# Kernel tuning notes

Hardware: AMD Instinct MI355X
Metric: run time of the kernel (lower is better)

Reference implementation:

```python
import jax, jax.numpy as jnp
import numpy as np

HIDDEN = 256
MAX_LENGTH = 256
NUM_LAYERS = 4
VOCAB = 50257


def setup_inputs() -> dict:
    key = jax.random.key(0)
    ks = jax.random.split(key, 16)
    s = 0.05
    return {
        "token": jax.random.randint(ks[0], (1,), 0, VOCAB, dtype=jnp.int64 if jax.config.jax_enable_x64 else jnp.int32),
        "hidden": jax.random.normal(ks[1], (NUM_LAYERS, 1, HIDDEN), dtype=jnp.float32),
        "encoder_outputs": jax.random.normal(ks[2], (MAX_LENGTH, HIDDEN), dtype=jnp.float32),
        "emb": jax.random.normal(ks[3], (VOCAB, HIDDEN), dtype=jnp.float32) * s,
        "attn_w": jax.random.normal(ks[4], (MAX_LENGTH, 2 * HIDDEN), dtype=jnp.float32) * s,
        "attn_b": jax.random.normal(ks[5], (MAX_LENGTH,), dtype=jnp.float32) * s,
        "comb_w": jax.random.normal(ks[6], (HIDDEN, 2 * HIDDEN), dtype=jnp.float32) * s,
        "comb_b": jax.random.normal(ks[7], (HIDDEN,), dtype=jnp.float32) * s,
        "gru_wih": jax.random.normal(ks[8], (NUM_LAYERS, 3 * HIDDEN, HIDDEN), dtype=jnp.float32) * s,
        "gru_whh": jax.random.normal(ks[9], (NUM_LAYERS, 3 * HIDDEN, HIDDEN), dtype=jnp.float32) * s,
        "gru_bih": jax.random.normal(ks[10], (NUM_LAYERS, 3 * HIDDEN), dtype=jnp.float32) * s,
        "gru_bhh": jax.random.normal(ks[11], (NUM_LAYERS, 3 * HIDDEN), dtype=jnp.float32) * s,
        "out_w": jax.random.normal(ks[12], (VOCAB, HIDDEN), dtype=jnp.float32) * s,
        "out_b": jax.random.normal(ks[13], (VOCAB,), dtype=jnp.float32) * s,
    }


def _gru_cell(x, h, wih, whh, bih, bhh):
    # PyTorch GRU cell: gates ordered [r, z, n]
    gi = x @ wih.T + bih  # [1, 3H]
    gh = h @ whh.T + bhh  # [1, 3H]
    i_r, i_z, i_n = jnp.split(gi, 3, axis=1)
    h_r, h_z, h_n = jnp.split(gh, 3, axis=1)
    r = jax.nn.sigmoid(i_r + h_r)
    z = jax.nn.sigmoid(i_z + h_z)
    n = jnp.tanh(i_n + r * h_n)
    return (1.0 - z) * n + z * h


def reference(token, hidden, encoder_outputs, emb, attn_w, attn_b, comb_w, comb_b,
              gru_wih, gru_whh, gru_bih, gru_bhh, out_w, out_b):
    # embedding lookup (dropout is identity in eval)  -> [1, H]
    embedded = emb[token]
    # Bahdanau-style attention weights over MAX_LENGTH positions
    attn_in = jnp.concatenate([embedded, hidden[0]], axis=1)  # [1, 2H]
    attn_weights = jax.nn.softmax(attn_in @ attn_w.T + attn_b, axis=1)  # [1, L]
    attn_applied = attn_weights @ encoder_outputs  # [1, H]
    comb_in = jnp.concatenate([embedded, attn_applied], axis=1)  # [1, 2H]
    x = jax.nn.relu(comb_in @ comb_w.T + comb_b)  # [1, H]
    # 4-layer GRU, single timestep
    new_h = []
    for l in range(NUM_LAYERS):
        h_l = _gru_cell(x, hidden[l], gru_wih[l], gru_whh[l], gru_bih[l], gru_bhh[l])
        new_h.append(h_l)
        x = h_l
    hidden_new = jnp.stack(new_h, axis=0)  # [4, 1, H]
    logp = jax.nn.log_softmax(x @ out_w.T + out_b, axis=1)  # [1, V]
    return (logp, hidden_new, attn_weights)
```

## Files before the change

### kernel.cpp

```cpp
#include <hip/hip_runtime.h>
#include <hip/hip_bf16.h>

#define H 256
#define L2H 512
#define NLAYERS 4
#define VOCAB 50257

#define OUT_LOGP 0
#define OUT_HID  50257
#define OUT_ATTN 51281

#define WS_SCORE  0
#define WS_BARS   256
#define WS_APP    512
#define WS_X0     768
#define WS_X1     1024
#define WS_PM     1280
#define WS_PS     1792
#define WS_FLAG   2304

#define NBLK 256
#define NGRP 16

typedef unsigned short u16;

__device__ __forceinline__ float bf2f(u16 u) {
    return __uint_as_float(((unsigned int)u) << 16);
}

__device__ __forceinline__ u16 f2bf(float f) {
    unsigned int x = __float_as_uint(f);
    unsigned int r = x + 0x7fff + ((x >> 16) & 1);
    return (u16)(r >> 16);
}

template<bool BF16>
__device__ __forceinline__ float ld1(const void* p, size_t i) {
    if (BF16) return bf2f(((const u16*)p)[i]);
    else      return ((const float*)p)[i];
}

template<bool BF16>
__device__ __forceinline__ float4 ld4(const void* p, size_t i) {
    if (BF16) {
        ushort4 w = *(const ushort4*)((const u16*)p + i);
        return make_float4(bf2f(w.x), bf2f(w.y), bf2f(w.z), bf2f(w.w));
    } else {
        return *(const float4*)((const float*)p + i);
    }
}

template<bool BF16>
__device__ __forceinline__ void ld8(const void* p, size_t i, float* f) {
    if (BF16) {
        uint4 u = *(const uint4*)((const u16*)p + i);
        f[0] = bf2f(u.x & 0xffff); f[1] = bf2f(u.x >> 16);
        f[2] = bf2f(u.y & 0xffff); f[3] = bf2f(u.y >> 16);
        f[4] = bf2f(u.z & 0xffff); f[5] = bf2f(u.z >> 16);
        f[6] = bf2f(u.w & 0xffff); f[7] = bf2f(u.w >> 16);
    } else {
        const float4* q = (const float4*)((const float*)p + i);
        float4 a = q[0], b = q[1];
        f[0] = a.x; f[1] = a.y; f[2] = a.z; f[3] = a.w;
        f[4] = b.x; f[5] = b.y; f[6] = b.z; f[7] = b.w;
    }
}

template<bool BF16>
__device__ __forceinline__ void st(void* p, size_t i, float v) {
    if (BF16) ((u16*)p)[i] = f2bf(v);
    else      ((float*)p)[i] = v;
}

__device__ __forceinline__ float ldc(const float* p) {
    return __hip_atomic_load(const_cast<float*>(p), __ATOMIC_RELAXED, __HIP_MEMORY_SCOPE_AGENT);
}
__device__ __forceinline__ void stc(float* p, float v) {
    __hip_atomic_store(p, v, __ATOMIC_RELAXED, __HIP_MEMORY_SCOPE_AGENT);
}

__device__ __forceinline__ void gbar(unsigned* bars, int i, bool arrive, unsigned exp) {
    __syncthreads();
    if (arrive && threadIdx.x == 0)
        __hip_atomic_fetch_add(&bars[(blockIdx.x & (NGRP - 1)) * 16 + i], 1u,
                               __ATOMIC_RELAXED, __HIP_MEMORY_SCOPE_AGENT);
    if (threadIdx.x < NGRP) {
        while (__hip_atomic_load(&bars[threadIdx.x * 16 + i],
                                 __ATOMIC_RELAXED, __HIP_MEMORY_SCOPE_AGENT) < exp)
            __builtin_amdgcn_s_sleep(1);
    }
    __syncthreads();
}

__global__ __launch_bounds__(256) void k_init(const void* emb, float* ws) {
    int tid = threadIdx.x;
    ((unsigned*)(ws + WS_BARS))[tid] = 0u;
    ws[WS_APP + tid] = 0.f;
    if (tid < 64) {
        float b = fabsf(bf2f(((const u16*)emb)[tid]));
        #pragma unroll
        for (int off = 32; off; off >>= 1) b = fmaxf(b, __shfl_xor(b, off));
        if (tid == 0) ws[WS_FLAG] = (b < 1.0f) ? 1.0f : 0.0f;
    }
}

template<bool BF16>
__device__ __forceinline__ void pipeline(
    const int* __restrict__ tok, const void* __restrict__ emb,
    const void* __restrict__ hidden,
    const void* __restrict__ attn_w, const void* __restrict__ attn_b,
    const void* __restrict__ enc,
    const void* __restrict__ comb_w, const void* __restrict__ comb_b,
    const void* __restrict__ gwih, const void* __restrict__ gwhh,
    const void* __restrict__ gbih, const void* __restrict__ gbhh,
    const void* __restrict__ out_w, const void* __restrict__ out_b,
    float* __restrict__ ws, void* __restrict__ out)
{
    unsigned* bars = (unsigned*)(ws + WS_BARS);
    const int tid  = threadIdx.x;
    const int lane = tid & 63;
    const int wid  = tid >> 6;
    const int bx   = blockIdx.x;
    const size_t es = BF16 ? 2 : 4;

    __shared__ float lds[256];
    __shared__ float wsm[256];

    if (bx < 64) {
        const int wv = (bx << 2) | wid;
        const int j8 = lane * 8;

        {
            float xin[8];
            if (lane < 32) ld8<BF16>(emb, (size_t)tok[0] * H + j8, xin);
            else           ld8<BF16>(hidden, (size_t)(j8 - H), xin);
            float wf[8]; ld8<BF16>(attn_w, (size_t)wv * L2H + j8, wf);
            float v = 0.f;
            #pragma unroll
            for (int q = 0; q < 8; ++q) v += xin[q] * wf[q];
            #pragma unroll
            for (int off = 32; off; off >>= 1) v += __shfl_xor(v, off);
            if (lane == 0) stc(ws + WS_SCORE + wv, v + ld1<BF16>(attn_b, wv));
        }
        gbar(bars, 0, true, 4);

        if (bx < 16) {
            float s = ldc(ws + WS_SCORE + tid);
            lds[tid] = s; __syncthreads();
            for (int off = 128; off; off >>= 1) {
                if (tid < off) lds[tid] = fmaxf(lds[tid], lds[tid + off]);
                __syncthreads();
            }
            float M = lds[0]; __syncthreads();
            float e = __expf(s - M);
            lds[tid] = e; __syncthreads();
            for (int off = 128; off; off >>= 1) {
                if (tid < off) lds[tid] += lds[tid + off];
                __syncthreads();
            }
            float w = e / lds[0];
            wsm[tid] = w; __syncthreads();
            if (bx == 0) st<BF16>(out, OUT_ATTN + tid, w);
            int l0 = bx * 16;
            float acc = 0.f;
            #pragma unroll
            for (int k = 0; k < 16; ++k)
                acc += wsm[l0 + k] * ld1<BF16>(enc, (size_t)(l0 + k) * H + tid);
            atomicAdd(&ws[WS_APP + tid], acc);
        }
        gbar(bars, 1, true, 4);

        {
            float xin[8];
            if (lane < 32) {
                ld8<BF16>(emb, (size_t)tok[0] * H + j8, xin);
            } else {
                #pragma unroll
                for (int q = 0; q < 8; ++q) xin[q] = ldc(ws + WS_APP + (j8 - H) + q);
            }
            float wf[8]; ld8<BF16>(comb_w, (size_t)wv * L2H + j8, wf);
            float v = 0.f;
            #pragma unroll
            for (int q = 0; q < 8; ++q) v += xin[q] * wf[q];
            #pragma unroll
            for (int off = 32; off; off >>= 1) v += __shfl_xor(v, off);
            if (lane == 0) stc(ws + WS_X0 + wv, fmaxf(v + ld1<BF16>(comb_b, wv), 0.f));
        }
        gbar(bars, 2, true, 4);

        const int e4 = lane * 4;
        for (int l = 0; l < NLAYERS; ++l) {
            const float* xin_p = ws + ((l & 1) ? WS_X1 : WS_X0);
            float*       xout  = ws + ((l & 1) ? WS_X0 : WS_X1);
            const char* wih = (const char*)gwih + (size_t)l * 3 * H * H * es;
            const char* whh = (const char*)gwhh + (size_t)l * 3 * H * H * es;
            const char* bih = (const char*)gbih + (size_t)l * 3 * H * es;
            const char* bhh = (const char*)gbhh + (size_t)l * 3 * H * es;
            const char* hprev = (const char*)hidden + (size_t)l * H * es;
            char*       hout  = (char*)out + (size_t)(OUT_HID + l * H) * es;

            float4 xv;
            xv.x = ldc(xin_p + e4);     xv.y = ldc(xin_p + e4 + 1);
            xv.z = ldc(xin_p + e4 + 2); xv.w = ldc(xin_p + e4 + 3);
            float4 hv = ld4<BF16>(hprev, e4);
            const int i = wv;

            float4 wri = ld4<BF16>(wih, (size_t)(i        ) * H + e4);
            float4 wzi = ld4<BF16>(wih, (size_t)(H + i    ) * H + e4);
            float4 wni = ld4<BF16>(wih, (size_t)(2 * H + i) * H + e4);
            float4 wrh = ld4<BF16>(whh, (size_t)(i        ) * H + e4);
            float4 wzh = ld4<BF16>(whh, (size_t)(H + i    ) * H + e4);
            float4 wnh = ld4<BF16>(whh, (size_t)(2 * H + i) * H + e4);

            float a = wri.x * xv.x + wri.y * xv.y + wri.z * xv.z + wri.w * xv.w
                    + wrh.x * hv.x + wrh.y * hv.y + wrh.z * hv.z + wrh.w * hv.w;
            float b = wzi.x * xv.x + wzi.y * xv.y + wzi.z * xv.z + wzi.w * xv.w
                    + wzh.x * hv.x + wzh.y * hv.y + wzh.z * hv.z + wzh.w * hv.w;
            float c = wni.x * xv.x + wni.y * xv.y + wni.z * xv.z + wni.w * xv.w;
            float d = wnh.x * hv.x + wnh.y * hv.y + wnh.z * hv.z + wnh.w * hv.w;

            #pragma unroll
            for (int off = 32; off; off >>= 1) {
                a += __shfl_xor(a, off);
                b += __shfl_xor(b, off);
                c += __shfl_xor(c, off);
                d += __shfl_xor(d, off);
            }
            if (lane == 0) {
                float r = 1.f / (1.f + __expf(-(a + ld1<BF16>(bih, i) + ld1<BF16>(bhh, i))));
                float z = 1.f / (1.f + __expf(-(b + ld1<BF16>(bih, H + i) + ld1<BF16>(bhh, H + i))));
                float n = tanhf(c + ld1<BF16>(bih, 2 * H + i) + r * (d + ld1<BF16>(bhh, 2 * H + i)));
                float hold = ld1<BF16>(hprev, i);
                float hn = (1.f - z) * n + z * hold;
                stc(xout + i, hn);
                st<BF16>(hout, i, hn);
            }
            gbar(bars, 3 + l, true, 4);
        }
    } else {
        gbar(bars, 6, false, 4);
    }

    {
        const int grp = (bx << 3) | (tid >> 5);
        const int l32 = tid & 31;

        float xf[8];
        #pragma unroll
        for (int q = 0; q < 8; ++q) xf[q] = ldc(ws + WS_X0 + l32 * 8 + q);

        float m = -1e30f, s = 0.f;
        #pragma unroll
        for (int it = 0; it < 3; ++it) {
            const int rb = it * 16384 + grp;
            float wf[8][8], bb[8];
            #pragma unroll
            for (int k = 0; k < 8; ++k) {
                ld8<BF16>(out_w, (size_t)(rb + (k << 11)) * H + l32 * 8, wf[k]);
                bb[k] = ld1<BF16>(out_b, rb + (k << 11));
            }
            #pragma unroll
            for (int k = 0; k < 8; ++k) {
                float v = wf[k][0]*xf[0] + wf[k][1]*xf[1] + wf[k][2]*xf[2] + wf[k][3]*xf[3]
                        + wf[k][4]*xf[4] + wf[k][5]*xf[5] + wf[k][6]*xf[6] + wf[k][7]*xf[7];
                #pragma unroll
                for (int off = 16; off; off >>= 1) v += __shfl_xor(v, off);
                v += bb[k];
                if (l32 == 0) st<BF16>(out, OUT_LOGP + rb + (k << 11), v);
                float mn = fmaxf(m, v);
                s = s * __expf(m - mn) + __expf(v - mn);
                m = mn;
            }
        }
        if (grp < VOCAB - 49152) {
            int r = 49152 + grp;
            float wf[8]; ld8<BF16>(out_w, (size_t)r * H + l32 * 8, wf);
            float v = wf[0]*xf[0] + wf[1]*xf[1] + wf[2]*xf[2] + wf[3]*xf[3]
                    + wf[4]*xf[4] + wf[5]*xf[5] + wf[6]*xf[6] + wf[7]*xf[7];
            #pragma unroll
            for (int off = 16; off; off >>= 1) v += __shfl_xor(v, off);
            v += ld1<BF16>(out_b, r);
            if (l32 == 0) st<BF16>(out, OUT_LOGP + r, v);
            float mn = fmaxf(m, v);
            s = s * __expf(m - mn) + __expf(v - mn);
            m = mn;
        }

        {
            float mo = __shfl_xor(m, 32), so = __shfl_xor(s, 32);
            float M = fmaxf(m, mo);
            s = s * __expf(m - M) + so * __expf(mo - M);
            m = M;
        }
        if (lane == 0) { lds[wid] = m; lds[4 + wid] = s; }
        __syncthreads();
        if (tid == 0) {
            float M01 = fmaxf(lds[0], lds[1]);
            float S01 = lds[4] * __expf(lds[0] - M01) + lds[5] * __expf(lds[1] - M01);
            float M23 = fmaxf(lds[2], lds[3]);
            float S23 = lds[6] * __expf(lds[2] - M23) + lds[7] * __expf(lds[3] - M23);
            float Mx = fmaxf(M01, M23);
            float S  = S01 * __expf(M01 - Mx) + S23 * __expf(M23 - Mx);
            stc(ws + WS_PM + bx, Mx);
            stc(ws + WS_PS + bx, S);
        }
    }
    gbar(bars, 7, true, 16);

    {
        float m = ldc(ws + WS_PM + tid);
        float s = ldc(ws + WS_PS + tid);
        #pragma unroll
        for (int off = 32; off; off >>= 1) {
            float mo = __shfl_xor(m, off), so = __shfl_xor(s, off);
            float M = fmaxf(m, mo);
            s = s * __expf(m - M) + so * __expf(mo - M);
            m = M;
        }
        if (lane == 0) { lds[wid] = m; lds[4 + wid] = s; }
        __syncthreads();
        if (tid == 0) {
            float M01 = fmaxf(lds[0], lds[1]);
            float S01 = lds[4] * __expf(lds[0] - M01) + lds[5] * __expf(lds[1] - M01);
            float M23 = fmaxf(lds[2], lds[3]);
            float S23 = lds[6] * __expf(lds[2] - M23) + lds[7] * __expf(lds[3] - M23);
            float Mx = fmaxf(M01, M23);
            float S  = S01 * __expf(M01 - Mx) + S23 * __expf(M23 - Mx);
            lds[8] = Mx + __logf(S);
        }
        __syncthreads();
        float c = lds[8];
        const int grp = (bx << 3) | (tid >> 5);
        const int j   = tid & 31;
        int r = ((j >> 3) << 14) + ((j & 7) << 11) + grp;
        if (r < VOCAB) {
            float v = ld1<BF16>(out, OUT_LOGP + r);
            st<BF16>(out, OUT_LOGP + r, v - c);
        }
    }
}

__global__ __launch_bounds__(256, 1) void k_all(
    const int* __restrict__ tok, const void* __restrict__ emb,
    const void* __restrict__ hidden,
    const void* __restrict__ attn_w, const void* __restrict__ attn_b,
    const void* __restrict__ enc,
    const void* __restrict__ comb_w, const void* __restrict__ comb_b,
    const void* __restrict__ gwih, const void* __restrict__ gwhh,
    const void* __restrict__ gbih, const void* __restrict__ gbhh,
    const void* __restrict__ out_w, const void* __restrict__ out_b,
    float* __restrict__ ws, void* __restrict__ out)
{
    if (ws[WS_FLAG] > 0.5f)
        pipeline<true >(tok, emb, hidden, attn_w, attn_b, enc, comb_w, comb_b,
                        gwih, gwhh, gbih, gbhh, out_w, out_b, ws, out);
    else
        pipeline<false>(tok, emb, hidden, attn_w, attn_b, enc, comb_w, comb_b,
                        gwih, gwhh, gbih, gbhh, out_w, out_b, ws, out);
}

extern "C" void kernel_launch(void* const* d_in, const int* in_sizes, int n_in,
                              void* d_out, int out_size, void* d_ws, size_t ws_size,
                              hipStream_t stream) {
    const int* tok = (const int*)d_in[0];
    float* ws = (float*)d_ws;

    k_init<<<dim3(1), dim3(256), 0, stream>>>(d_in[3], ws);
    k_all<<<dim3(NBLK), dim3(256), 0, stream>>>(
        tok, d_in[3], d_in[1], d_in[4], d_in[5], d_in[2], d_in[6], d_in[7],
        d_in[8], d_in[9], d_in[10], d_in[11], d_in[12], d_in[13],
        ws, d_out);
}
```

Baseline: 170.4 us.

## Split grid barriers into arrive/wait counters and keep logits in registers

Replaces the grouped full-grid barrier with per-stage counters. Producers arrive and consumers spin only on the stage they depend on, so weight and encoder loads are issued before the wait and overlap the barrier latency. The idle blocks no longer pass through the pipeline barriers and go straight to waiting for the final GRU output. Logits are kept in registers instead of being written and read back for the log-softmax shift, which removes one global round trip. The cost is 25 extra registers per thread and a single shared counter that all 256 blocks poll, which may contend.

```diff
diff --git a/kernel.cpp b/kernel.cpp
--- a/kernel.cpp
+++ b/kernel.cpp
@@ -20,7 +20,11 @@
 #define WS_FLAG   2304
 
 #define NBLK 256
-#define NGRP 16
+
+#define C_SCORE 0
+#define C_APP   1
+#define C_X(l)  (2 + (l))
+#define C_LOG   7
 
 typedef unsigned short u16;
 
@@ -79,15 +83,15 @@
     __hip_atomic_store(p, v, __ATOMIC_RELAXED, __HIP_MEMORY_SCOPE_AGENT);
 }
 
-__device__ __forceinline__ void gbar(unsigned* bars, int i, bool arrive, unsigned exp) {
+__device__ __forceinline__ void arrive(unsigned* bars, int i) {
     __syncthreads();
-    if (arrive && threadIdx.x == 0)
-        __hip_atomic_fetch_add(&bars[(blockIdx.x & (NGRP - 1)) * 16 + i], 1u,
-                               __ATOMIC_RELAXED, __HIP_MEMORY_SCOPE_AGENT);
-    if (threadIdx.x < NGRP) {
-        while (__hip_atomic_load(&bars[threadIdx.x * 16 + i],
-                                 __ATOMIC_RELAXED, __HIP_MEMORY_SCOPE_AGENT) < exp)
-            __builtin_amdgcn_s_sleep(1);
+    if (threadIdx.x == 0)
+        __hip_atomic_fetch_add(&bars[i * 16], 1u, __ATOMIC_RELAXED, __HIP_MEMORY_SCOPE_AGENT);
+}
+__device__ __forceinline__ void wait_for(unsigned* bars, int i, unsigned exp) {
+    if (threadIdx.x == 0) {
+        while (__hip_atomic_load(&bars[i * 16], __ATOMIC_RELAXED, __HIP_MEMORY_SCOPE_AGENT) < exp)
+            __builtin_amdgcn_s_sleep(2);
     }
     __syncthreads();
 }
@@ -142,9 +146,15 @@
             for (int off = 32; off; off >>= 1) v += __shfl_xor(v, off);
             if (lane == 0) stc(ws + WS_SCORE + wv, v + ld1<BF16>(attn_b, wv));
         }
-        gbar(bars, 0, true, 4);
+        arrive(bars, C_SCORE);
 
         if (bx < 16) {
+            const int l0 = bx * 16;
+            float ev[16];
+            #pragma unroll
+            for (int k = 0; k < 16; ++k)
+                ev[k] = ld1<BF16>(enc, (size_t)(l0 + k) * H + tid);
+            wait_for(bars, C_SCORE, 64);
             float s = ldc(ws + WS_SCORE + tid);
             lds[tid] = s; __syncthreads();
             for (int off = 128; off; off >>= 1) {
@@ -161,24 +171,22 @@
             float w = e / lds[0];
             wsm[tid] = w; __syncthreads();
             if (bx == 0) st<BF16>(out, OUT_ATTN + tid, w);
-            int l0 = bx * 16;
             float acc = 0.f;
             #pragma unroll
-            for (int k = 0; k < 16; ++k)
-                acc += wsm[l0 + k] * ld1<BF16>(enc, (size_t)(l0 + k) * H + tid);
+            for (int k = 0; k < 16; ++k) acc += wsm[l0 + k] * ev[k];
             atomicAdd(&ws[WS_APP + tid], acc);
-        }
-        gbar(bars, 1, true, 4);
+            arrive(bars, C_APP);
+        }
 
         {
+            float wf[8]; ld8<BF16>(comb_w, (size_t)wv * L2H + j8, wf);
             float xin[8];
-            if (lane < 32) {
-                ld8<BF16>(emb, (size_t)tok[0] * H + j8, xin);
-            } else {
+            if (lane < 32) ld8<BF16>(emb, (size_t)tok[0] * H + j8, xin);
+            wait_for(bars, C_APP, 16);
+            if (lane >= 32) {
                 #pragma unroll
                 for (int q = 0; q < 8; ++q) xin[q] = ldc(ws + WS_APP + (j8 - H) + q);
             }
-            float wf[8]; ld8<BF16>(comb_w, (size_t)wv * L2H + j8, wf);
             float v = 0.f;
             #pragma unroll
             for (int q = 0; q < 8; ++q) v += xin[q] * wf[q];
@@ -186,9 +194,10 @@
             for (int off = 32; off; off >>= 1) v += __shfl_xor(v, off);
             if (lane == 0) stc(ws + WS_X0 + wv, fmaxf(v + ld1<BF16>(comb_b, wv), 0.f));
         }
-        gbar(bars, 2, true, 4);
+        arrive(bars, C_X(0));
 
         const int e4 = lane * 4;
+        #pragma unroll 1
         for (int l = 0; l < NLAYERS; ++l) {
             const float* xin_p = ws + ((l & 1) ? WS_X1 : WS_X0);
             float*       xout  = ws + ((l & 1) ? WS_X0 : WS_X1);
@@ -198,19 +207,21 @@
             const char* bhh = (const char*)gbhh + (size_t)l * 3 * H * es;
             const char* hprev = (const char*)hidden + (size_t)l * H * es;
             char*       hout  = (char*)out + (size_t)(OUT_HID + l * H) * es;
-
-            float4 xv;
-            xv.x = ldc(xin_p + e4);     xv.y = ldc(xin_p + e4 + 1);
-            xv.z = ldc(xin_p + e4 + 2); xv.w = ldc(xin_p + e4 + 3);
-            float4 hv = ld4<BF16>(hprev, e4);
             const int i = wv;
 
+            float4 hv  = ld4<BF16>(hprev, e4);
             float4 wri = ld4<BF16>(wih, (size_t)(i        ) * H + e4);
             float4 wzi = ld4<BF16>(wih, (size_t)(H + i    ) * H + e4);
             float4 wni = ld4<BF16>(wih, (size_t)(2 * H + i) * H + e4);
             float4 wrh = ld4<BF16>(whh, (size_t)(i        ) * H + e4);
             float4 wzh = ld4<BF16>(whh, (size_t)(H + i    ) * H + e4);
             float4 wnh = ld4<BF16>(whh, (size_t)(2 * H + i) * H + e4);
+
+            wait_for(bars, C_X(l), 64);
+
+            float4 xv;
+            xv.x = ldc(xin_p + e4);     xv.y = ldc(xin_p + e4 + 1);
+            xv.z = ldc(xin_p + e4 + 2); xv.w = ldc(xin_p + e4 + 3);
 
             float a = wri.x * xv.x + wri.y * xv.y + wri.z * xv.z + wri.w * xv.w
                     + wrh.x * hv.x + wrh.y * hv.y + wrh.z * hv.z + wrh.w * hv.w;
@@ -235,16 +246,16 @@
                 stc(xout + i, hn);
                 st<BF16>(hout, i, hn);
             }
-            gbar(bars, 3 + l, true, 4);
-        }
-    } else {
-        gbar(bars, 6, false, 4);
-    }
-
+            arrive(bars, C_X(l + 1));
+        }
+    }
+
+    wait_for(bars, C_X(4), 64);
+
+    const int grp = (bx << 3) | (tid >> 5);
+    const int l32 = tid & 31;
+    float vs[25];
     {
-        const int grp = (bx << 3) | (tid >> 5);
-        const int l32 = tid & 31;
-
         float xf[8];
         #pragma unroll
         for (int q = 0; q < 8; ++q) xf[q] = ldc(ws + WS_X0 + l32 * 8 + q);
@@ -266,12 +277,13 @@
                 #pragma unroll
                 for (int off = 16; off; off >>= 1) v += __shfl_xor(v, off);
                 v += bb[k];
-                if (l32 == 0) st<BF16>(out, OUT_LOGP + rb + (k << 11), v);
+                vs[it * 8 + k] = v;
                 float mn = fmaxf(m, v);
                 s = s * __expf(m - mn) + __expf(v - mn);
                 m = mn;
             }
         }
+        vs[24] = 0.f;
         if (grp < VOCAB - 49152) {
             int r = 49152 + grp;
             float wf[8]; ld8<BF16>(out_w, (size_t)r * H + l32 * 8, wf);
@@ -280,7 +292,7 @@
             #pragma unroll
             for (int off = 16; off; off >>= 1) v += __shfl_xor(v, off);
             v += ld1<BF16>(out_b, r);
-            if (l32 == 0) st<BF16>(out, OUT_LOGP + r, v);
+            vs[24] = v;
             float mn = fmaxf(m, v);
             s = s * __expf(m - mn) + __expf(v - mn);
             m = mn;
@@ -305,7 +317,8 @@
             stc(ws + WS_PS + bx, S);
         }
     }
-    gbar(bars, 7, true, 16);
+    arrive(bars, C_LOG);
+    wait_for(bars, C_LOG, 256);
 
     {
         float m = ldc(ws + WS_PM + tid);
@@ -330,12 +343,15 @@
         }
         __syncthreads();
         float c = lds[8];
-        const int grp = (bx << 3) | (tid >> 5);
-        const int j   = tid & 31;
-        int r = ((j >> 3) << 14) + ((j & 7) << 11) + grp;
-        if (r < VOCAB) {
-            float v = ld1<BF16>(out, OUT_LOGP + r);
-            st<BF16>(out, OUT_LOGP + r, v - c);
+        if (l32 == 0) {
+            #pragma unroll
+            for (int it = 0; it < 3; ++it) {
+                #pragma unroll
+                for (int k = 0; k < 8; ++k)
+                    st<BF16>(out, OUT_LOGP + it * 16384 + (k << 11) + grp, vs[it * 8 + k] - c);
+            }
+            if (grp < VOCAB - 49152)
+                st<BF16>(out, OUT_LOGP + 49152 + grp, vs[24] - c);
         }
     }
 }
```

New measurement: 174.0 us. 1.02x slower.
